# Kernel optimization log

Measured on AMD Instinct MI355X. Metric: run time of the kernel, lower is better.

The kernel has to match this reference:

```python
import jax, jax.numpy as jnp
import numpy as np

N_NODES = 100000
FEAT_DIM = 128
EMBED_DIM = 128
NUM_SAMPLE = 10


def setup_inputs() -> dict:
    key = jax.random.key(0)
    k1, k2, k3, k4, k5 = jax.random.split(key, 5)
    features = jax.random.normal(k1, (N_NODES, FEAT_DIM), dtype=jnp.float32)
    W1 = jax.random.normal(k2, (EMBED_DIM, FEAT_DIM), dtype=jnp.float32) * (1.0 / np.sqrt(FEAT_DIM))
    W2 = jax.random.normal(k3, (EMBED_DIM, EMBED_DIM), dtype=jnp.float32) * (1.0 / np.sqrt(EMBED_DIM))
    adj = jax.random.randint(k4, (N_NODES, NUM_SAMPLE), 0, N_NODES, dtype=jnp.int64)
    nodes = jax.random.randint(k5, (N_NODES,), 0, N_NODES, dtype=jnp.int64)
    return {"features": features, "W1": W1, "W2": W2, "adj": adj, "nodes": nodes}


def reference(features, W1, W2, adj, nodes):
    # 2-layer GraphSAGE with gcn=True: mean over {self} U sampled neighbors,
    # then relu(agg @ W.T). Layer 1 is computed for all nodes since layer 2
    # needs embeddings of arbitrary neighbors.
    n = features.shape[0]
    self_idx = jnp.arange(n, dtype=adj.dtype)[:, None]            # [N,1]
    neigh1 = jnp.concatenate([self_idx, adj], axis=1)             # [N,S+1]
    agg1 = jnp.mean(features[neigh1], axis=1)                     # [N,F] (gather+mean)
    h1 = jax.nn.relu(agg1 @ W1.T)                                 # [N,E]

    neigh2 = jnp.concatenate([nodes[:, None], adj[nodes]], axis=1)  # [B,S+1]
    agg2 = jnp.mean(h1[neigh2], axis=1)                           # [B,E]
    out = jax.nn.relu(agg2 @ W2.T).T                              # [E,B], Encoder returns embed_dim x num_nodes
    return out
```

## Files before the change

kernel.cpp:

```cpp
#include <hip/hip_runtime.h>

#define N_NODES 100000
#define DIM 128
#define NS 10
#define SCALE (1.0f / 11.0f)

typedef unsigned int uint;
typedef unsigned short ushort;
typedef __attribute__((ext_vector_type(8))) short bf16x8;
typedef __attribute__((ext_vector_type(4))) float f32x4;

__device__ inline float bl(uint u) {
    union { uint x; float f; } c; c.x = u << 16; return c.f;
}
__device__ inline uint f2b(float x) {
    union { float f; uint u; } c; c.f = x;
    return (c.u + 0x7FFFu + ((c.u >> 16) & 1u)) >> 16;
}

__global__ __launch_bounds__(256) void wsplit(const float* __restrict__ W1,
                                              const float* __restrict__ W2,
                                              ushort* __restrict__ o) {
    const int i = blockIdx.x * 256 + threadIdx.x;
    const float a = W1[i];
    uint h = f2b(a);
    o[i] = (ushort)h;
    o[16384 + i] = (ushort)f2b(a - bl(h));
    const float b = W2[i];
    h = f2b(b);
    o[32768 + i] = (ushort)h;
    o[49152 + i] = (ushort)f2b(b - bl(h));
}

__global__ __launch_bounds__(256, 2) void gemm1(const float* __restrict__ X,
                                                const ushort* __restrict__ Whi,
                                                const ushort* __restrict__ Wlo,
                                                ushort* __restrict__ C) {
    __shared__ __align__(16) ushort lds[8192];
    const int t = threadIdx.x;
    const int lane = t & 63;
    const int wave = t >> 6;
    const int m16 = lane & 15;
    const int kq = lane >> 4;
    const int r0 = blockIdx.x * 32;

    const int v0 = t, v1 = t + 256;
    const int ln0 = v0 & 63, ln1 = v1 & 63;
    const float* s0 = X + (size_t)(r0 + (v0 >> 8) * 16 + (ln0 & 15)) * DIM +
                      ((v0 >> 6) & 3) * 32 + (ln0 >> 4) * 8;
    const float* s1 = X + (size_t)(r0 + (v1 >> 8) * 16 + (ln1 & 15)) * DIM +
                      ((v1 >> 6) & 3) * 32 + (ln1 >> 4) * 8;
    const float4 f00 = *(const float4*)(s0);
    const float4 f01 = *(const float4*)(s0 + 4);
    const float4 f10 = *(const float4*)(s1);
    const float4 f11 = *(const float4*)(s1 + 4);

    bf16x8 wh[2][4], wl[2][4];
#pragma unroll
    for (int c = 0; c < 2; ++c)
#pragma unroll
        for (int ks = 0; ks < 4; ++ks) {
            const size_t off = (size_t)((2 * wave + c) * 16 + m16) * DIM + ks * 32 + kq * 8;
            wh[c][ks] = *(const bf16x8*)(Whi + off);
            wl[c][ks] = *(const bf16x8*)(Wlo + off);
        }

    {
        const float xs[8] = {f00.x, f00.y, f00.z, f00.w, f01.x, f01.y, f01.z, f01.w};
        bf16x8 hi, lo;
#pragma unroll
        for (int j = 0; j < 8; ++j) {
            const uint hb = f2b(xs[j]);
            hi[j] = (short)hb;
            lo[j] = (short)f2b(xs[j] - bl(hb));
        }
        *(bf16x8*)(lds + (v0 >> 6) * 512 + ln0 * 8) = hi;
        *(bf16x8*)(lds + 4096 + (v0 >> 6) * 512 + ln0 * 8) = lo;
    }
    {
        const float xs[8] = {f10.x, f10.y, f10.z, f10.w, f11.x, f11.y, f11.z, f11.w};
        bf16x8 hi, lo;
#pragma unroll
        for (int j = 0; j < 8; ++j) {
            const uint hb = f2b(xs[j]);
            hi[j] = (short)hb;
            lo[j] = (short)f2b(xs[j] - bl(hb));
        }
        *(bf16x8*)(lds + (v1 >> 6) * 512 + ln1 * 8) = hi;
        *(bf16x8*)(lds + 4096 + (v1 >> 6) * 512 + ln1 * 8) = lo;
    }
    __syncthreads();

    f32x4 acc[2][2];
#pragma unroll
    for (int bt = 0; bt < 2; ++bt)
#pragma unroll
        for (int c = 0; c < 2; ++c) acc[bt][c] = (f32x4){0.f, 0.f, 0.f, 0.f};

#pragma unroll
    for (int ks = 0; ks < 4; ++ks) {
#pragma unroll
        for (int bt = 0; bt < 2; ++bt) {
            const int g = bt * 4 + ks;
            const bf16x8 xh = *(const bf16x8*)(lds + g * 512 + lane * 8);
            const bf16x8 xl = *(const bf16x8*)(lds + 4096 + g * 512 + lane * 8);
#pragma unroll
            for (int c = 0; c < 2; ++c) {
                acc[bt][c] = __builtin_amdgcn_mfma_f32_16x16x32_bf16(wh[c][ks], xh, acc[bt][c], 0, 0, 0);
                acc[bt][c] = __builtin_amdgcn_mfma_f32_16x16x32_bf16(wl[c][ks], xh, acc[bt][c], 0, 0, 0);
                acc[bt][c] = __builtin_amdgcn_mfma_f32_16x16x32_bf16(wh[c][ks], xl, acc[bt][c], 0, 0, 0);
            }
        }
    }

#pragma unroll
    for (int bt = 0; bt < 2; ++bt) {
        const size_t row = (size_t)(r0 + bt * 16 + m16);
#pragma unroll
        for (int c = 0; c < 2; ++c) {
            uint2 w;
            w.x = f2b(acc[bt][c][0]) | (f2b(acc[bt][c][1]) << 16);
            w.y = f2b(acc[bt][c][2]) | (f2b(acc[bt][c][3]) << 16);
            *(uint2*)(C + row * DIM + (2 * wave + c) * 16 + kq * 4) = w;
        }
    }
}

__global__ __launch_bounds__(256) void agg1(const ushort* __restrict__ FW,
                                            const int* __restrict__ adj,
                                            ushort* __restrict__ H) {
    __shared__ int idx_lds[320];
    const int t = threadIdx.x;
    const int r0 = blockIdx.x * 32;
    for (int l = t; l < 320; l += 256)
        idx_lds[l] = adj[(size_t)r0 * NS + l];
    __syncthreads();
    const int team = t >> 4;
    const int j = t & 15;
#pragma unroll
    for (int rp = 0; rp < 2; ++rp) {
        const int ri = team * 2 + rp;
        const int row = r0 + ri;
        uint4 u[11];
        u[0] = *(const uint4*)(FW + (size_t)row * DIM + j * 8);
#pragma unroll
        for (int s = 0; s < NS; ++s)
            u[1 + s] = *(const uint4*)(FW + (size_t)idx_lds[ri * NS + s] * DIM + j * 8);
        float a[8];
#pragma unroll
        for (int k = 0; k < 8; ++k) a[k] = 0.f;
#pragma unroll
        for (int s = 0; s < 11; ++s) {
            a[0] += bl(u[s].x); a[1] += bl(u[s].x >> 16);
            a[2] += bl(u[s].y); a[3] += bl(u[s].y >> 16);
            a[4] += bl(u[s].z); a[5] += bl(u[s].z >> 16);
            a[6] += bl(u[s].w); a[7] += bl(u[s].w >> 16);
        }
        uint4 w;
        w.x = f2b(fmaxf(a[0] * SCALE, 0.f)) | (f2b(fmaxf(a[1] * SCALE, 0.f)) << 16);
        w.y = f2b(fmaxf(a[2] * SCALE, 0.f)) | (f2b(fmaxf(a[3] * SCALE, 0.f)) << 16);
        w.z = f2b(fmaxf(a[4] * SCALE, 0.f)) | (f2b(fmaxf(a[5] * SCALE, 0.f)) << 16);
        w.w = f2b(fmaxf(a[6] * SCALE, 0.f)) | (f2b(fmaxf(a[7] * SCALE, 0.f)) << 16);
        *(uint4*)(H + (size_t)row * DIM + j * 8) = w;
    }
}

__global__ __launch_bounds__(256) void agg2b(const ushort* __restrict__ H,
                                             const int* __restrict__ adj,
                                             const int* __restrict__ nodes,
                                             ushort* __restrict__ P) {
    __shared__ int idx_lds[32 * 11];
    const int t = threadIdx.x;
    const int r0 = blockIdx.x * 32;
    if (t < 32) idx_lds[t * 11] = nodes[r0 + t];
    __syncthreads();
    for (int l = t; l < 320; l += 256) {
        const int bi = l / 10;
        const int s = l - bi * 10;
        idx_lds[bi * 11 + 1 + s] = adj[(size_t)idx_lds[bi * 11] * NS + s];
    }
    __syncthreads();
    const int team = t >> 4;
    const int j = t & 15;
#pragma unroll
    for (int rp = 0; rp < 2; ++rp) {
        const int ri = team * 2 + rp;
        uint4 u[11];
#pragma unroll
        for (int s = 0; s < 11; ++s)
            u[s] = *(const uint4*)(H + (size_t)idx_lds[ri * 11 + s] * DIM + j * 8);
        float a[8];
#pragma unroll
        for (int k = 0; k < 8; ++k) a[k] = 0.f;
#pragma unroll
        for (int s = 0; s < 11; ++s) {
            a[0] += bl(u[s].x); a[1] += bl(u[s].x >> 16);
            a[2] += bl(u[s].y); a[3] += bl(u[s].y >> 16);
            a[4] += bl(u[s].z); a[5] += bl(u[s].z >> 16);
            a[6] += bl(u[s].w); a[7] += bl(u[s].w >> 16);
        }
        uint4 w;
        w.x = f2b(a[0] * SCALE) | (f2b(a[1] * SCALE) << 16);
        w.y = f2b(a[2] * SCALE) | (f2b(a[3] * SCALE) << 16);
        w.z = f2b(a[4] * SCALE) | (f2b(a[5] * SCALE) << 16);
        w.w = f2b(a[6] * SCALE) | (f2b(a[7] * SCALE) << 16);
        *(uint4*)(P + (size_t)(r0 + ri) * DIM + j * 8) = w;
    }
}

__global__ __launch_bounds__(256, 2) void gemm2t(const ushort* __restrict__ P,
                                                 const ushort* __restrict__ Whi,
                                                 const ushort* __restrict__ Wlo,
                                                 float* __restrict__ out) {
    __shared__ __align__(16) ushort lds[4096];
    const int t = threadIdx.x;
    const int lane = t & 63;
    const int wave = t >> 6;
    const int m16 = lane & 15;
    const int kq = lane >> 4;
    const int r0 = blockIdx.x * 32;

    const int v0 = t, v1 = t + 256;
    const int ln0 = v0 & 63, ln1 = v1 & 63;
    const ushort* s0 = P + (size_t)(r0 + (v0 >> 8) * 16 + (ln0 & 15)) * DIM +
                       ((v0 >> 6) & 3) * 32 + (ln0 >> 4) * 8;
    const ushort* s1 = P + (size_t)(r0 + (v1 >> 8) * 16 + (ln1 & 15)) * DIM +
                       ((v1 >> 6) & 3) * 32 + (ln1 >> 4) * 8;
    const bf16x8 p0 = *(const bf16x8*)(s0);
    const bf16x8 p1 = *(const bf16x8*)(s1);

    bf16x8 wh[2][4], wl[2][4];
#pragma unroll
    for (int c = 0; c < 2; ++c)
#pragma unroll
        for (int ks = 0; ks < 4; ++ks) {
            const size_t off = (size_t)((2 * wave + c) * 16 + m16) * DIM + ks * 32 + kq * 8;
            wh[c][ks] = *(const bf16x8*)(Whi + off);
            wl[c][ks] = *(const bf16x8*)(Wlo + off);
        }

    *(bf16x8*)(lds + (v0 >> 6) * 512 + ln0 * 8) = p0;
    *(bf16x8*)(lds + (v1 >> 6) * 512 + ln1 * 8) = p1;
    __syncthreads();

    f32x4 acc[2][2];
#pragma unroll
    for (int bt = 0; bt < 2; ++bt)
#pragma unroll
        for (int c = 0; c < 2; ++c) acc[bt][c] = (f32x4){0.f, 0.f, 0.f, 0.f};

#pragma unroll
    for (int ks = 0; ks < 4; ++ks) {
#pragma unroll
        for (int bt = 0; bt < 2; ++bt) {
            const bf16x8 pa = *(const bf16x8*)(lds + (bt * 4 + ks) * 512 + lane * 8);
#pragma unroll
            for (int c = 0; c < 2; ++c) {
                acc[bt][c] = __builtin_amdgcn_mfma_f32_16x16x32_bf16(pa, wh[c][ks], acc[bt][c], 0, 0, 0);
                acc[bt][c] = __builtin_amdgcn_mfma_f32_16x16x32_bf16(pa, wl[c][ks], acc[bt][c], 0, 0, 0);
            }
        }
    }

#pragma unroll
    for (int bt = 0; bt < 2; ++bt) {
        const int b = r0 + bt * 16 + kq * 4;
#pragma unroll
        for (int c = 0; c < 2; ++c) {
            const int e = (2 * wave + c) * 16 + m16;
            float4 v;
            v.x = fmaxf(acc[bt][c][0], 0.f);
            v.y = fmaxf(acc[bt][c][1], 0.f);
            v.z = fmaxf(acc[bt][c][2], 0.f);
            v.w = fmaxf(acc[bt][c][3], 0.f);
            *(float4*)(out + (size_t)e * N_NODES + b) = v;
        }
    }
}

extern "C" void kernel_launch(void* const* d_in, const int* in_sizes, int n_in,
                              void* d_out, int out_size, void* d_ws, size_t ws_size,
                              hipStream_t stream) {
    const float* features = (const float*)d_in[0];
    const float* W1 = (const float*)d_in[1];
    const float* W2 = (const float*)d_in[2];
    const int* adj = (const int*)d_in[3];
    const int* nodes = (const int*)d_in[4];
    float* out = (float*)d_out;

    const size_t NE = (size_t)N_NODES * DIM;
    ushort* fw = (ushort*)d_ws;
    ushort* h1 = fw + NE;
    ushort* wpl = h1 + NE;
    ushort* w1hi = wpl;
    ushort* w1lo = wpl + 16384;
    ushort* w2hi = wpl + 32768;
    ushort* w2lo = wpl + 49152;

    wsplit<<<64, 256, 0, stream>>>(W1, W2, wpl);
    gemm1<<<N_NODES / 32, 256, 0, stream>>>(features, w1hi, w1lo, fw);
    agg1<<<N_NODES / 32, 256, 0, stream>>>(fw, adj, h1);
    agg2b<<<N_NODES / 32, 256, 0, stream>>>(h1, adj, nodes, fw);
    gemm2t<<<N_NODES / 32, 256, 0, stream>>>(fw, w2hi, w2lo, out);
}
```

Before: 155.1 us.

## Split bf16 feature matrices into two 64-column planes for cache-friendly gathers

The intermediate bf16 matrices (FW, H, P) are stored as two separate planes of 64 columns each instead of one 128-column row-major array. The gather kernels process one plane at a time across all rows, so each random gather touches a 128-byte row slice and the working set per pass is halved, which should improve L2/MALL hit rates for the random neighbor accesses. The GEMM producer and consumer are updated to the split addressing. Each thread now issues narrower 8-byte loads and twice as many passes, which may lower memory-level parallelism per load.

```diff
diff --git a/kernel.cpp b/kernel.cpp
--- a/kernel.cpp
+++ b/kernel.cpp
@@ -4,6 +4,7 @@
 #define DIM 128
 #define NS 10
 #define SCALE (1.0f / 11.0f)
+#define NE2 ((size_t)N_NODES * 64)
 
 typedef unsigned int uint;
 typedef unsigned short ushort;
@@ -121,7 +122,8 @@
             uint2 w;
             w.x = f2b(acc[bt][c][0]) | (f2b(acc[bt][c][1]) << 16);
             w.y = f2b(acc[bt][c][2]) | (f2b(acc[bt][c][3]) << 16);
-            *(uint2*)(C + row * DIM + (2 * wave + c) * 16 + kq * 4) = w;
+            *(uint2*)(C + (size_t)(wave >> 1) * NE2 + row * 64 +
+                      (2 * (wave & 1) + c) * 16 + kq * 4) = w;
         }
     }
 }
@@ -137,31 +139,36 @@
     __syncthreads();
     const int team = t >> 4;
     const int j = t & 15;
-#pragma unroll
-    for (int rp = 0; rp < 2; ++rp) {
-        const int ri = team * 2 + rp;
-        const int row = r0 + ri;
-        uint4 u[11];
-        u[0] = *(const uint4*)(FW + (size_t)row * DIM + j * 8);
+    const int ri0 = team * 2, ri1 = team * 2 + 1;
+#pragma unroll
+    for (int p = 0; p < 2; ++p) {
+        const ushort* FWp = FW + (size_t)p * NE2;
+        ushort* Hp = H + (size_t)p * NE2;
+        uint2 u0[11], u1[11];
+        u0[0] = ((const uint2*)(FWp + (size_t)(r0 + ri0) * 64))[j];
 #pragma unroll
         for (int s = 0; s < NS; ++s)
-            u[1 + s] = *(const uint4*)(FW + (size_t)idx_lds[ri * NS + s] * DIM + j * 8);
-        float a[8];
-#pragma unroll
-        for (int k = 0; k < 8; ++k) a[k] = 0.f;
+            u0[1 + s] = ((const uint2*)(FWp + (size_t)idx_lds[ri0 * NS + s] * 64))[j];
+        u1[0] = ((const uint2*)(FWp + (size_t)(r0 + ri1) * 64))[j];
+#pragma unroll
+        for (int s = 0; s < NS; ++s)
+            u1[1 + s] = ((const uint2*)(FWp + (size_t)idx_lds[ri1 * NS + s] * 64))[j];
+        float a0 = 0.f, a1 = 0.f, a2 = 0.f, a3 = 0.f;
+        float b0 = 0.f, b1 = 0.f, b2 = 0.f, b3 = 0.f;
 #pragma unroll
         for (int s = 0; s < 11; ++s) {
-            a[0] += bl(u[s].x); a[1] += bl(u[s].x >> 16);
-            a[2] += bl(u[s].y); a[3] += bl(u[s].y >> 16);
-            a[4] += bl(u[s].z); a[5] += bl(u[s].z >> 16);
-            a[6] += bl(u[s].w); a[7] += bl(u[s].w >> 16);
-        }
-        uint4 w;
-        w.x = f2b(fmaxf(a[0] * SCALE, 0.f)) | (f2b(fmaxf(a[1] * SCALE, 0.f)) << 16);
-        w.y = f2b(fmaxf(a[2] * SCALE, 0.f)) | (f2b(fmaxf(a[3] * SCALE, 0.f)) << 16);
-        w.z = f2b(fmaxf(a[4] * SCALE, 0.f)) | (f2b(fmaxf(a[5] * SCALE, 0.f)) << 16);
-        w.w = f2b(fmaxf(a[6] * SCALE, 0.f)) | (f2b(fmaxf(a[7] * SCALE, 0.f)) << 16);
-        *(uint4*)(H + (size_t)row * DIM + j * 8) = w;
+            a0 += bl(u0[s].x); a1 += bl(u0[s].x >> 16);
+            a2 += bl(u0[s].y); a3 += bl(u0[s].y >> 16);
+            b0 += bl(u1[s].x); b1 += bl(u1[s].x >> 16);
+            b2 += bl(u1[s].y); b3 += bl(u1[s].y >> 16);
+        }
+        uint2 w;
+        w.x = f2b(fmaxf(a0 * SCALE, 0.f)) | (f2b(fmaxf(a1 * SCALE, 0.f)) << 16);
+        w.y = f2b(fmaxf(a2 * SCALE, 0.f)) | (f2b(fmaxf(a3 * SCALE, 0.f)) << 16);
+        ((uint2*)(Hp + (size_t)(r0 + ri0) * 64))[j] = w;
+        w.x = f2b(fmaxf(b0 * SCALE, 0.f)) | (f2b(fmaxf(b1 * SCALE, 0.f)) << 16);
+        w.y = f2b(fmaxf(b2 * SCALE, 0.f)) | (f2b(fmaxf(b3 * SCALE, 0.f)) << 16);
+        ((uint2*)(Hp + (size_t)(r0 + ri1) * 64))[j] = w;
     }
 }
 
@@ -182,29 +189,34 @@
     __syncthreads();
     const int team = t >> 4;
     const int j = t & 15;
-#pragma unroll
-    for (int rp = 0; rp < 2; ++rp) {
-        const int ri = team * 2 + rp;
-        uint4 u[11];
+    const int ri0 = team * 2, ri1 = team * 2 + 1;
+#pragma unroll
+    for (int p = 0; p < 2; ++p) {
+        const ushort* Hp = H + (size_t)p * NE2;
+        ushort* Pp = P + (size_t)p * NE2;
+        uint2 u0[11], u1[11];
 #pragma unroll
         for (int s = 0; s < 11; ++s)
-            u[s] = *(const uint4*)(H + (size_t)idx_lds[ri * 11 + s] * DIM + j * 8);
-        float a[8];
-#pragma unroll
-        for (int k = 0; k < 8; ++k) a[k] = 0.f;
+            u0[s] = ((const uint2*)(Hp + (size_t)idx_lds[ri0 * 11 + s] * 64))[j];
+#pragma unroll
+        for (int s = 0; s < 11; ++s)
+            u1[s] = ((const uint2*)(Hp + (size_t)idx_lds[ri1 * 11 + s] * 64))[j];
+        float a0 = 0.f, a1 = 0.f, a2 = 0.f, a3 = 0.f;
+        float b0 = 0.f, b1 = 0.f, b2 = 0.f, b3 = 0.f;
 #pragma unroll
         for (int s = 0; s < 11; ++s) {
-            a[0] += bl(u[s].x); a[1] += bl(u[s].x >> 16);
-            a[2] += bl(u[s].y); a[3] += bl(u[s].y >> 16);
-            a[4] += bl(u[s].z); a[5] += bl(u[s].z >> 16);
-            a[6] += bl(u[s].w); a[7] += bl(u[s].w >> 16);
-        }
-        uint4 w;
-        w.x = f2b(a[0] * SCALE) | (f2b(a[1] * SCALE) << 16);
-        w.y = f2b(a[2] * SCALE) | (f2b(a[3] * SCALE) << 16);
-        w.z = f2b(a[4] * SCALE) | (f2b(a[5] * SCALE) << 16);
-        w.w = f2b(a[6] * SCALE) | (f2b(a[7] * SCALE) << 16);
-        *(uint4*)(P + (size_t)(r0 + ri) * DIM + j * 8) = w;
+            a0 += bl(u0[s].x); a1 += bl(u0[s].x >> 16);
+            a2 += bl(u0[s].y); a3 += bl(u0[s].y >> 16);
+            b0 += bl(u1[s].x); b1 += bl(u1[s].x >> 16);
+            b2 += bl(u1[s].y); b3 += bl(u1[s].y >> 16);
+        }
+        uint2 w;
+        w.x = f2b(a0 * SCALE) | (f2b(a1 * SCALE) << 16);
+        w.y = f2b(a2 * SCALE) | (f2b(a3 * SCALE) << 16);
+        ((uint2*)(Pp + (size_t)(r0 + ri0) * 64))[j] = w;
+        w.x = f2b(b0 * SCALE) | (f2b(b1 * SCALE) << 16);
+        w.y = f2b(b2 * SCALE) | (f2b(b3 * SCALE) << 16);
+        ((uint2*)(Pp + (size_t)(r0 + ri1) * 64))[j] = w;
     }
 }
 
@@ -222,10 +234,13 @@
 
     const int v0 = t, v1 = t + 256;
     const int ln0 = v0 & 63, ln1 = v1 & 63;
-    const ushort* s0 = P + (size_t)(r0 + (v0 >> 8) * 16 + (ln0 & 15)) * DIM +
-                       ((v0 >> 6) & 3) * 32 + (ln0 >> 4) * 8;
-    const ushort* s1 = P + (size_t)(r0 + (v1 >> 8) * 16 + (ln1 & 15)) * DIM +
-                       ((v1 >> 6) & 3) * 32 + (ln1 >> 4) * 8;
+    const int ksq0 = (v0 >> 6) & 3, ksq1 = (v1 >> 6) & 3;
+    const ushort* s0 = P + (size_t)(ksq0 >> 1) * NE2 +
+                       (size_t)(r0 + (v0 >> 8) * 16 + (ln0 & 15)) * 64 +
+                       (ksq0 & 1) * 32 + (ln0 >> 4) * 8;
+    const ushort* s1 = P + (size_t)(ksq1 >> 1) * NE2 +
+                       (size_t)(r0 + (v1 >> 8) * 16 + (ln1 & 15)) * 64 +
+                       (ksq1 & 1) * 32 + (ln1 >> 4) * 8;
     const bf16x8 p0 = *(const bf16x8*)(s0);
     const bf16x8 p1 = *(const bf16x8*)(s1);
 
```

After: 154.7 us. Within noise of the previous version (-0.3%).

## Strip-major feature layout for gathers, fuse weight split and index prep

Applied to the files above, without the earlier changes.

Intermediate buffers are stored as 8 column strips of 16 bf16 values per node. Each aggregation block handles one strip for 128 nodes, so the random gathers of all blocks sharing a strip stay within a 3.2 MB region that is more likely to hit cache. The separate weight-split kernel is removed and each GEMM block splits W into hi/lo bf16 in registers itself. The two-hop index list for layer 2 is precomputed inside gemm1 and written to workspace, which removes the dependent nodes-to-adj lookup from agg2b at the cost of extra per-block weight conversion and index writes.

```diff
diff --git a/kernel.cpp b/kernel.cpp
--- a/kernel.cpp
+++ b/kernel.cpp
@@ -4,6 +4,9 @@
 #define DIM 128
 #define NS 10
 #define SCALE (1.0f / 11.0f)
+#define N16 ((size_t)N_NODES * 16)
+#define NSTRIP 3125
+#define NAGG 6256
 
 typedef unsigned int uint;
 typedef unsigned short ushort;
@@ -17,25 +20,24 @@
     union { float f; uint u; } c; c.f = x;
     return (c.u + 0x7FFFu + ((c.u >> 16) & 1u)) >> 16;
 }
-
-__global__ __launch_bounds__(256) void wsplit(const float* __restrict__ W1,
-                                              const float* __restrict__ W2,
-                                              ushort* __restrict__ o) {
-    const int i = blockIdx.x * 256 + threadIdx.x;
-    const float a = W1[i];
-    uint h = f2b(a);
-    o[i] = (ushort)h;
-    o[16384 + i] = (ushort)f2b(a - bl(h));
-    const float b = W2[i];
-    h = f2b(b);
-    o[32768 + i] = (ushort)h;
-    o[49152 + i] = (ushort)f2b(b - bl(h));
+__device__ inline void split8(const float* __restrict__ p, bf16x8& h, bf16x8& l) {
+    const float4 a = *(const float4*)p;
+    const float4 b = *(const float4*)(p + 4);
+    const float xs[8] = {a.x, a.y, a.z, a.w, b.x, b.y, b.z, b.w};
+#pragma unroll
+    for (int j = 0; j < 8; ++j) {
+        const uint hb = f2b(xs[j]);
+        h[j] = (short)hb;
+        l[j] = (short)f2b(xs[j] - bl(hb));
+    }
 }
 
 __global__ __launch_bounds__(256, 2) void gemm1(const float* __restrict__ X,
-                                                const ushort* __restrict__ Whi,
-                                                const ushort* __restrict__ Wlo,
-                                                ushort* __restrict__ C) {
+                                                const float* __restrict__ W1,
+                                                const int* __restrict__ adj,
+                                                const int* __restrict__ nodes,
+                                                ushort* __restrict__ C,
+                                                int* __restrict__ idx2) {
     __shared__ __align__(16) ushort lds[8192];
     const int t = threadIdx.x;
     const int lane = t & 63;
@@ -44,50 +46,40 @@
     const int kq = lane >> 4;
     const int r0 = blockIdx.x * 32;
 
+    bf16x8 wh[2][4], wl[2][4];
+#pragma unroll
+    for (int c = 0; c < 2; ++c)
+#pragma unroll
+        for (int ks = 0; ks < 4; ++ks)
+            split8(W1 + (size_t)((2 * wave + c) * 16 + m16) * DIM + ks * 32 + kq * 8,
+                   wh[c][ks], wl[c][ks]);
+
     const int v0 = t, v1 = t + 256;
     const int ln0 = v0 & 63, ln1 = v1 & 63;
-    const float* s0 = X + (size_t)(r0 + (v0 >> 8) * 16 + (ln0 & 15)) * DIM +
-                      ((v0 >> 6) & 3) * 32 + (ln0 >> 4) * 8;
-    const float* s1 = X + (size_t)(r0 + (v1 >> 8) * 16 + (ln1 & 15)) * DIM +
-                      ((v1 >> 6) & 3) * 32 + (ln1 >> 4) * 8;
-    const float4 f00 = *(const float4*)(s0);
-    const float4 f01 = *(const float4*)(s0 + 4);
-    const float4 f10 = *(const float4*)(s1);
-    const float4 f11 = *(const float4*)(s1 + 4);
-
-    bf16x8 wh[2][4], wl[2][4];
-#pragma unroll
-    for (int c = 0; c < 2; ++c)
-#pragma unroll
-        for (int ks = 0; ks < 4; ++ks) {
-            const size_t off = (size_t)((2 * wave + c) * 16 + m16) * DIM + ks * 32 + kq * 8;
-            wh[c][ks] = *(const bf16x8*)(Whi + off);
-            wl[c][ks] = *(const bf16x8*)(Wlo + off);
-        }
-
     {
-        const float xs[8] = {f00.x, f00.y, f00.z, f00.w, f01.x, f01.y, f01.z, f01.w};
+        const float* s0 = X + (size_t)(r0 + (v0 >> 8) * 16 + (ln0 & 15)) * DIM +
+                          ((v0 >> 6) & 3) * 32 + (ln0 >> 4) * 8;
         bf16x8 hi, lo;
-#pragma unroll
-        for (int j = 0; j < 8; ++j) {
-            const uint hb = f2b(xs[j]);
-            hi[j] = (short)hb;
-            lo[j] = (short)f2b(xs[j] - bl(hb));
-        }
+        split8(s0, hi, lo);
         *(bf16x8*)(lds + (v0 >> 6) * 512 + ln0 * 8) = hi;
         *(bf16x8*)(lds + 4096 + (v0 >> 6) * 512 + ln0 * 8) = lo;
     }
     {
-        const float xs[8] = {f10.x, f10.y, f10.z, f10.w, f11.x, f11.y, f11.z, f11.w};
+        const float* s1 = X + (size_t)(r0 + (v1 >> 8) * 16 + (ln1 & 15)) * DIM +
+                          ((v1 >> 6) & 3) * 32 + (ln1 >> 4) * 8;
         bf16x8 hi, lo;
-#pragma unroll
-        for (int j = 0; j < 8; ++j) {
-            const uint hb = f2b(xs[j]);
-            hi[j] = (short)hb;
-            lo[j] = (short)f2b(xs[j] - bl(hb));
-        }
+        split8(s1, hi, lo);
         *(bf16x8*)(lds + (v1 >> 6) * 512 + ln1 * 8) = hi;
         *(bf16x8*)(lds + 4096 + (v1 >> 6) * 512 + ln1 * 8) = lo;
+    }
+
+    if (t < 32) {
+        const int r = r0 + t;
+        const int n = nodes[r];
+        idx2[(size_t)r * 11] = n;
+#pragma unroll
+        for (int s = 0; s < NS; ++s)
+            idx2[(size_t)r * 11 + 1 + s] = adj[(size_t)n * NS + s];
     }
     __syncthreads();
 
@@ -121,7 +113,7 @@
             uint2 w;
             w.x = f2b(acc[bt][c][0]) | (f2b(acc[bt][c][1]) << 16);
             w.y = f2b(acc[bt][c][2]) | (f2b(acc[bt][c][3]) << 16);
-            *(uint2*)(C + row * DIM + (2 * wave + c) * 16 + kq * 4) = w;
+            *(uint2*)(C + (size_t)(2 * wave + c) * N16 + row * 16 + kq * 4) = w;
         }
     }
 }
@@ -129,88 +121,84 @@
 __global__ __launch_bounds__(256) void agg1(const ushort* __restrict__ FW,
                                             const int* __restrict__ adj,
                                             ushort* __restrict__ H) {
-    __shared__ int idx_lds[320];
-    const int t = threadIdx.x;
-    const int r0 = blockIdx.x * 32;
-    for (int l = t; l < 320; l += 256)
-        idx_lds[l] = adj[(size_t)r0 * NS + l];
-    __syncthreads();
-    const int team = t >> 4;
-    const int j = t & 15;
-#pragma unroll
-    for (int rp = 0; rp < 2; ++rp) {
-        const int ri = team * 2 + rp;
-        const int row = r0 + ri;
-        uint4 u[11];
-        u[0] = *(const uint4*)(FW + (size_t)row * DIM + j * 8);
-#pragma unroll
-        for (int s = 0; s < NS; ++s)
-            u[1 + s] = *(const uint4*)(FW + (size_t)idx_lds[ri * NS + s] * DIM + j * 8);
-        float a[8];
-#pragma unroll
-        for (int k = 0; k < 8; ++k) a[k] = 0.f;
-#pragma unroll
-        for (int s = 0; s < 11; ++s) {
-            a[0] += bl(u[s].x); a[1] += bl(u[s].x >> 16);
-            a[2] += bl(u[s].y); a[3] += bl(u[s].y >> 16);
-            a[4] += bl(u[s].z); a[5] += bl(u[s].z >> 16);
-            a[6] += bl(u[s].w); a[7] += bl(u[s].w >> 16);
-        }
-        uint4 w;
-        w.x = f2b(fmaxf(a[0] * SCALE, 0.f)) | (f2b(fmaxf(a[1] * SCALE, 0.f)) << 16);
-        w.y = f2b(fmaxf(a[2] * SCALE, 0.f)) | (f2b(fmaxf(a[3] * SCALE, 0.f)) << 16);
-        w.z = f2b(fmaxf(a[4] * SCALE, 0.f)) | (f2b(fmaxf(a[5] * SCALE, 0.f)) << 16);
-        w.w = f2b(fmaxf(a[6] * SCALE, 0.f)) | (f2b(fmaxf(a[7] * SCALE, 0.f)) << 16);
-        *(uint4*)(H + (size_t)row * DIM + j * 8) = w;
-    }
+    __shared__ int idx[1280];
+    const int t = threadIdx.x;
+    const int s = blockIdx.x & 7;
+    const int r0 = (blockIdx.x >> 3) * 128;
+    for (int l = t; l < 1280; l += 256) {
+        const size_t gi = (size_t)r0 * NS + l;
+        idx[l] = (gi < (size_t)N_NODES * NS) ? adj[gi] : 0;
+    }
+    __syncthreads();
+    const int ri = t >> 1;
+    const int hf = t & 1;
+    const int row = r0 + ri;
+    if (row >= N_NODES) return;
+    const ushort* Fp = FW + (size_t)s * N16 + hf * 8;
+    uint4 u[11];
+    u[0] = *(const uint4*)(Fp + (size_t)row * 16);
+#pragma unroll
+    for (int q = 0; q < NS; ++q)
+        u[1 + q] = *(const uint4*)(Fp + (size_t)idx[ri * NS + q] * 16);
+    float a[8];
+#pragma unroll
+    for (int k = 0; k < 8; ++k) a[k] = 0.f;
+#pragma unroll
+    for (int q = 0; q < 11; ++q) {
+        a[0] += bl(u[q].x); a[1] += bl(u[q].x >> 16);
+        a[2] += bl(u[q].y); a[3] += bl(u[q].y >> 16);
+        a[4] += bl(u[q].z); a[5] += bl(u[q].z >> 16);
+        a[6] += bl(u[q].w); a[7] += bl(u[q].w >> 16);
+    }
+    uint4 w;
+    w.x = f2b(fmaxf(a[0] * SCALE, 0.f)) | (f2b(fmaxf(a[1] * SCALE, 0.f)) << 16);
+    w.y = f2b(fmaxf(a[2] * SCALE, 0.f)) | (f2b(fmaxf(a[3] * SCALE, 0.f)) << 16);
+    w.z = f2b(fmaxf(a[4] * SCALE, 0.f)) | (f2b(fmaxf(a[5] * SCALE, 0.f)) << 16);
+    w.w = f2b(fmaxf(a[6] * SCALE, 0.f)) | (f2b(fmaxf(a[7] * SCALE, 0.f)) << 16);
+    *(uint4*)(H + (size_t)s * N16 + (size_t)row * 16 + hf * 8) = w;
 }
 
 __global__ __launch_bounds__(256) void agg2b(const ushort* __restrict__ H,
-                                             const int* __restrict__ adj,
-                                             const int* __restrict__ nodes,
+                                             const int* __restrict__ idx2,
                                              ushort* __restrict__ P) {
-    __shared__ int idx_lds[32 * 11];
-    const int t = threadIdx.x;
-    const int r0 = blockIdx.x * 32;
-    if (t < 32) idx_lds[t * 11] = nodes[r0 + t];
-    __syncthreads();
-    for (int l = t; l < 320; l += 256) {
-        const int bi = l / 10;
-        const int s = l - bi * 10;
-        idx_lds[bi * 11 + 1 + s] = adj[(size_t)idx_lds[bi * 11] * NS + s];
-    }
-    __syncthreads();
-    const int team = t >> 4;
-    const int j = t & 15;
-#pragma unroll
-    for (int rp = 0; rp < 2; ++rp) {
-        const int ri = team * 2 + rp;
-        uint4 u[11];
-#pragma unroll
-        for (int s = 0; s < 11; ++s)
-            u[s] = *(const uint4*)(H + (size_t)idx_lds[ri * 11 + s] * DIM + j * 8);
-        float a[8];
-#pragma unroll
-        for (int k = 0; k < 8; ++k) a[k] = 0.f;
-#pragma unroll
-        for (int s = 0; s < 11; ++s) {
-            a[0] += bl(u[s].x); a[1] += bl(u[s].x >> 16);
-            a[2] += bl(u[s].y); a[3] += bl(u[s].y >> 16);
-            a[4] += bl(u[s].z); a[5] += bl(u[s].z >> 16);
-            a[6] += bl(u[s].w); a[7] += bl(u[s].w >> 16);
-        }
-        uint4 w;
-        w.x = f2b(a[0] * SCALE) | (f2b(a[1] * SCALE) << 16);
-        w.y = f2b(a[2] * SCALE) | (f2b(a[3] * SCALE) << 16);
-        w.z = f2b(a[4] * SCALE) | (f2b(a[5] * SCALE) << 16);
-        w.w = f2b(a[6] * SCALE) | (f2b(a[7] * SCALE) << 16);
-        *(uint4*)(P + (size_t)(r0 + ri) * DIM + j * 8) = w;
-    }
+    __shared__ int idx[1408];
+    const int t = threadIdx.x;
+    const int s = blockIdx.x & 7;
+    const int r0 = (blockIdx.x >> 3) * 128;
+    for (int l = t; l < 1408; l += 256) {
+        const size_t gi = (size_t)r0 * 11 + l;
+        idx[l] = (gi < (size_t)N_NODES * 11) ? idx2[gi] : 0;
+    }
+    __syncthreads();
+    const int ri = t >> 1;
+    const int hf = t & 1;
+    const int row = r0 + ri;
+    if (row >= N_NODES) return;
+    const ushort* Hp = H + (size_t)s * N16 + hf * 8;
+    uint4 u[11];
+#pragma unroll
+    for (int q = 0; q < 11; ++q)
+        u[q] = *(const uint4*)(Hp + (size_t)idx[ri * 11 + q] * 16);
+    float a[8];
+#pragma unroll
+    for (int k = 0; k < 8; ++k) a[k] = 0.f;
+#pragma unroll
+    for (int q = 0; q < 11; ++q) {
+        a[0] += bl(u[q].x); a[1] += bl(u[q].x >> 16);
+        a[2] += bl(u[q].y); a[3] += bl(u[q].y >> 16);
+        a[4] += bl(u[q].z); a[5] += bl(u[q].z >> 16);
+        a[6] += bl(u[q].w); a[7] += bl(u[q].w >> 16);
+    }
+    uint4 w;
+    w.x = f2b(a[0] * SCALE) | (f2b(a[1] * SCALE) << 16);
+    w.y = f2b(a[2] * SCALE) | (f2b(a[3] * SCALE) << 16);
+    w.z = f2b(a[4] * SCALE) | (f2b(a[5] * SCALE) << 16);
+    w.w = f2b(a[6] * SCALE) | (f2b(a[7] * SCALE) << 16);
+    *(uint4*)(P + (size_t)s * N16 + (size_t)row * 16 + hf * 8) = w;
 }
 
 __global__ __launch_bounds__(256, 2) void gemm2t(const ushort* __restrict__ P,
-                                                 const ushort* __restrict__ Whi,
-                                                 const ushort* __restrict__ Wlo,
+                                                 const float* __restrict__ W2,
                                                  float* __restrict__ out) {
     __shared__ __align__(16) ushort lds[4096];
     const int t = threadIdx.x;
@@ -220,27 +208,25 @@
     const int kq = lane >> 4;
     const int r0 = blockIdx.x * 32;
 
-    const int v0 = t, v1 = t + 256;
-    const int ln0 = v0 & 63, ln1 = v1 & 63;
-    const ushort* s0 = P + (size_t)(r0 + (v0 >> 8) * 16 + (ln0 & 15)) * DIM +
-                       ((v0 >> 6) & 3) * 32 + (ln0 >> 4) * 8;
-    const ushort* s1 = P + (size_t)(r0 + (v1 >> 8) * 16 + (ln1 & 15)) * DIM +
-                       ((v1 >> 6) & 3) * 32 + (ln1 >> 4) * 8;
-    const bf16x8 p0 = *(const bf16x8*)(s0);
-    const bf16x8 p1 = *(const bf16x8*)(s1);
+#pragma unroll
+    for (int i = 0; i < 2; ++i) {
+        const int v = t + i * 256;
+        const int ln = v & 63;
+        const int ksq = (v >> 6) & 3;
+        const int row = r0 + (v >> 8) * 16 + (ln & 15);
+        const int k0 = ksq * 32 + (ln >> 4) * 8;
+        const bf16x8 pv = *(const bf16x8*)(P + (size_t)(k0 >> 4) * N16 +
+                                           (size_t)row * 16 + (k0 & 15));
+        *(bf16x8*)(lds + (v >> 6) * 512 + ln * 8) = pv;
+    }
 
     bf16x8 wh[2][4], wl[2][4];
 #pragma unroll
     for (int c = 0; c < 2; ++c)
 #pragma unroll
-        for (int ks = 0; ks < 4; ++ks) {
-            const size_t off = (size_t)((2 * wave + c) * 16 + m16) * DIM + ks * 32 + kq * 8;
-            wh[c][ks] = *(const bf16x8*)(Whi + off);
-            wl[c][ks] = *(const bf16x8*)(Wlo + off);
-        }
-
-    *(bf16x8*)(lds + (v0 >> 6) * 512 + ln0 * 8) = p0;
-    *(bf16x8*)(lds + (v1 >> 6) * 512 + ln1 * 8) = p1;
+        for (int ks = 0; ks < 4; ++ks)
+            split8(W2 + (size_t)((2 * wave + c) * 16 + m16) * DIM + ks * 32 + kq * 8,
+                   wh[c][ks], wl[c][ks]);
     __syncthreads();
 
     f32x4 acc[2][2];
@@ -288,18 +274,13 @@
     const int* nodes = (const int*)d_in[4];
     float* out = (float*)d_out;
 
-    const size_t NE = (size_t)N_NODES * DIM;
     ushort* fw = (ushort*)d_ws;
-    ushort* h1 = fw + NE;
-    ushort* wpl = h1 + NE;
-    ushort* w1hi = wpl;
-    ushort* w1lo = wpl + 16384;
-    ushort* w2hi = wpl + 32768;
-    ushort* w2lo = wpl + 49152;
-
-    wsplit<<<64, 256, 0, stream>>>(W1, W2, wpl);
-    gemm1<<<N_NODES / 32, 256, 0, stream>>>(features, w1hi, w1lo, fw);
-    agg1<<<N_NODES / 32, 256, 0, stream>>>(fw, adj, h1);
-    agg2b<<<N_NODES / 32, 256, 0, stream>>>(h1, adj, nodes, fw);
-    gemm2t<<<N_NODES / 32, 256, 0, stream>>>(fw, w2hi, w2lo, out);
-}
+    ushort* h1 = fw + N16 * 8;
+    ushort* pp = h1 + N16 * 8;
+    int* idx2 = (int*)(pp + N16 * 8);
+
+    gemm1<<<NSTRIP, 256, 0, stream>>>(features, W1, adj, nodes, fw, idx2);
+    agg1<<<NAGG, 256, 0, stream>>>(fw, adj, h1);
+    agg2b<<<NAGG, 256, 0, stream>>>(h1, idx2, pp);
+    gemm2t<<<NSTRIP, 256, 0, stream>>>(pp, W2, out);
+}
```

Result: no change. 156.9 us (+1.2%).
